# Kernel optimization log

Hardware: AMD Instinct MI355X
Metric: run time of the kernel (lower is better)

## Reference

```python
import jax, jax.numpy as jnp
import numpy as np

N_NODES = 50000
NEG_SLOPE_ATT = 0.2   # PyG GATConv default LeakyReLU slope for attention logits
NEG_SLOPE_ACT = 0.01  # nn.LeakyReLU default between layers


def _add_self_loops(src, dst, n):
    loop = jnp.arange(n, dtype=src.dtype)
    return jnp.concatenate([src, loop]), jnp.concatenate([dst, loop])


def gat_conv(x, W, a_src, a_dst, b, src, dst, n):
    # x: [N, Cin], W: [Cin, Cout], a_src/a_dst: [Cout], b: [Cout]
    h = x @ W                                   # [N, Cout]
    alpha_src = h @ a_src                       # [N]
    alpha_dst = h @ a_dst                       # [N]
    e = jax.nn.leaky_relu(alpha_src[src] + alpha_dst[dst], NEG_SLOPE_ATT)  # [E]
    # segment softmax over incoming edges of each dst node
    m = jax.ops.segment_max(e, dst, num_segments=n)      # [N]
    ex = jnp.exp(e - m[dst])                              # [E]
    s = jax.ops.segment_sum(ex, dst, num_segments=n)      # [N] (>0: self-loops)
    alpha = ex / s[dst]                                   # [E]
    out = jax.ops.segment_sum(h[src] * alpha[:, None], dst, num_segments=n)
    return out + b


def setup_inputs() -> dict:
    key = jax.random.key(0)
    ks = jax.random.split(key, 20)
    n, e = N_NODES, 800000
    cin, h1, h2, cout = 64, 128, 64, 32
    d = {
        "x": jax.random.normal(ks[0], (n, cin), jnp.float32),
        "edge_index": jax.random.randint(ks[1], (2, e), 0, n, jnp.int64),
    }
    dims = [(cin, h1), (h1, h2), (h2, h1), (h1, cout)]
    for i, (ci, co) in enumerate(dims, 1):
        g = 1.0 / np.sqrt(ci)
        d[f"W{i}"] = jax.random.normal(ks[2 + 4 * i], (ci, co), jnp.float32) * g
        d[f"a{i}s"] = jax.random.normal(ks[3 + 4 * i], (co,), jnp.float32) * 0.1
        d[f"a{i}d"] = jax.random.normal(ks[4 + 4 * i], (co,), jnp.float32) * 0.1
        d[f"b{i}"] = jnp.zeros((co,), jnp.float32)
    return d


def reference(x, edge_index, W1, a1s, a1d, b1, W2, a2s, a2d, b2,
              W3, a3s, a3d, b3, W4, a4s, a4d, b4):
    n = x.shape[0]
    src, dst = _add_self_loops(edge_index[0], edge_index[1], n)
    act = lambda t: jax.nn.leaky_relu(t, NEG_SLOPE_ACT)
    h = act(gat_conv(x, W1, a1s, a1d, b1, src, dst, n))
    # dropout is identity at inference
    h = act(gat_conv(h, W2, a2s, a2d, b2, src, dst, n))
    h = act(gat_conv(h, W3, a3s, a3d, b3, src, dst, n))
    return gat_conv(h, W4, a4s, a4d, b4, src, dst, n)
```

## Files before the change

### kernel.cpp

```cpp
#include <hip/hip_runtime.h>

#define NEG_ATT 0.2f


__global__ __launch_bounds__(256) void count_k(const int* __restrict__ dst, int* cnt, int E, int step) {
    int part = blockIdx.x & 7;
    int i = (blockIdx.x >> 3) * 256 + threadIdx.x;
    int lo = part * step, hi = lo + step;
    if (i < E) {
        int d = dst[i];
        if (d >= lo && d < hi) atomicAdd(&cnt[d], 1);
    }
}

__global__ __launch_bounds__(256) void scan_block_k(const int* __restrict__ cnt, int* rowp, int* bsum, int N) {
    __shared__ int s[256];
    int t = threadIdx.x;
    int i = blockIdx.x * 256 + t;
    s[t] = (i < N) ? cnt[i] + 1 : 0;
    __syncthreads();
    #pragma unroll
    for (int off = 1; off < 256; off <<= 1) {
        int v = (t >= off) ? s[t - off] : 0;
        __syncthreads();
        s[t] += v;
        __syncthreads();
    }
    if (i < N) rowp[i + 1] = s[t];
    if (t == 255) bsum[blockIdx.x] = s[255];
}

__global__ void scan_bsum_k(int* bsum, int nb) {
    __shared__ int s[256];
    int t = threadIdx.x;
    s[t] = (t < nb) ? bsum[t] : 0;
    __syncthreads();
    if (t == 0) {
        int run = 0;
        for (int i = 0; i < nb; i++) { int v = s[i]; s[i] = run; run += v; }
    }
    __syncthreads();
    if (t < nb) bsum[t] = s[t];
}

__global__ __launch_bounds__(256) void add_off_k(int* rowp, const int* __restrict__ bsum, int* cnt, int N) {
    int i = blockIdx.x * 256 + threadIdx.x;
    if (i < N) { rowp[i + 1] += bsum[blockIdx.x]; cnt[i] = 0; }
    if (i == 0) rowp[0] = 0;
}

__global__ __launch_bounds__(256) void scatter_k(const int* __restrict__ src, const int* __restrict__ dst,
                                                 const int* __restrict__ rowp, int* cnt,
                                                 int* __restrict__ col, int E, int N, int step) {
    int part = blockIdx.x & 7;
    int i = (blockIdx.x >> 3) * 256 + threadIdx.x;
    int lo = part * step, hi = lo + step;
    if (i < E) {
        int d = dst[i];
        if (d >= lo && d < hi) {
            int p = rowp[d] + atomicAdd(&cnt[d], 1);
            col[p] = src[i];
        }
    } else if (i < E + N) {
        int d = i - E;
        if (d >= lo && d < hi) col[rowp[d + 1] - 1] = d;
    }
}


__global__ __launch_bounds__(256) void setup_k(int* cnt, int N, int NB,
                                               const float* __restrict__ W1, const float* __restrict__ a1s,
                                               const float* __restrict__ a1d, const float* __restrict__ W3,
                                               const float* __restrict__ a3s, const float* __restrict__ a3d,
                                               float* __restrict__ wa ) {
    int b = blockIdx.x;
    if (b < NB) {
        int i = b * 256 + threadIdx.x;
        if (i < N) cnt[i] = 0;
    } else {
        int t = threadIdx.x;
        int ci = t & 63;
        int which = t >> 6;
        const float* W = (which < 2) ? W1 : W3;
        const float* a = (which == 0) ? a1s : (which == 1) ? a1d : (which == 2) ? a3s : a3d;
        float s = 0.f;
        for (int co = 0; co < 128; ++co) s += W[ci * 128 + co] * a[co];
        wa[t] = s;
    }
}


__global__ __launch_bounds__(256) void gemv_k(const float* __restrict__ X, const float* __restrict__ was,
                                              const float* __restrict__ wad, float* __restrict__ as_,
                                              float* __restrict__ ad_, int N) {
    int wid  = (blockIdx.x * 256 + threadIdx.x) >> 6;
    int lane = threadIdx.x & 63;
    if (wid >= N) return;
    float xv = X[(size_t)wid * 64 + lane];
    float s1 = xv * was[lane];
    float s2 = xv * wad[lane];
    #pragma unroll
    for (int off = 32; off; off >>= 1) {
        s1 += __shfl_xor(s1, off);
        s2 += __shfl_xor(s2, off);
    }
    if (lane == 0) { as_[wid] = s1; ad_[wid] = s2; }
}


template <int CIN, int COUT, bool ATT, bool BIASACT>
__global__ __launch_bounds__(256) void gemm_k(const float* __restrict__ X, const float* __restrict__ W,
                                              const float* __restrict__ a_s, const float* __restrict__ a_d,
                                              const float* __restrict__ bias,
                                              float* __restrict__ H, float* __restrict__ as_,
                                              float* __restrict__ ad_, int N) {
    constexpr int RB  = (CIN == 128 && COUT == 64) ? 32 : 64;
    constexpr int NCT = COUT / 4;
    constexpr int NRT = 256 / NCT;
    constexpr int RT  = RB / NRT;
    constexpr int XP  = CIN + 4;
    __shared__ float Xs[RB][XP];
    __shared__ float Ws[CIN][COUT];
    int tid  = threadIdx.x;
    int row0 = blockIdx.x * RB;

    for (int i = tid; i < CIN * COUT / 4; i += 256)
        *(float4*)&((float*)Ws)[i * 4] = *(const float4*)&W[i * 4];
    for (int i = tid; i < RB * CIN / 4; i += 256) {
        int r = i / (CIN / 4), k4 = i % (CIN / 4);
        int gr = row0 + r;
        float4 v = {0.f, 0.f, 0.f, 0.f};
        if (gr < N) v = *(const float4*)&X[(size_t)gr * CIN + k4 * 4];
        *(float4*)&Xs[r][k4 * 4] = v;
    }
    __syncthreads();

    int ct = tid % NCT;
    int rt = tid / NCT;
    float acc[RT][4] = {};
    for (int k = 0; k < CIN; k += 4) {
        float4 w0 = *(float4*)&Ws[k][ct * 4];
        float4 w1 = *(float4*)&Ws[k + 1][ct * 4];
        float4 w2 = *(float4*)&Ws[k + 2][ct * 4];
        float4 w3 = *(float4*)&Ws[k + 3][ct * 4];
        #pragma unroll
        for (int i = 0; i < RT; ++i) {
            float4 xv = *(float4*)&Xs[rt + i * NRT][k];
            acc[i][0] += xv.x * w0.x + xv.y * w1.x + xv.z * w2.x + xv.w * w3.x;
            acc[i][1] += xv.x * w0.y + xv.y * w1.y + xv.z * w2.y + xv.w * w3.y;
            acc[i][2] += xv.x * w0.z + xv.y * w1.z + xv.z * w2.z + xv.w * w3.z;
            acc[i][3] += xv.x * w0.w + xv.y * w1.w + xv.z * w2.w + xv.w * w3.w;
        }
    }

    float asv[4], adv[4], bv[4];
    #pragma unroll
    for (int j = 0; j < 4; ++j) {
        if (ATT) { asv[j] = a_s[ct * 4 + j]; adv[j] = a_d[ct * 4 + j]; }
        if (BIASACT) bv[j] = bias[ct * 4 + j];
    }

    #pragma unroll
    for (int i = 0; i < RT; ++i) {
        int gr = row0 + rt + i * NRT;
        if (BIASACT) {
            #pragma unroll
            for (int j = 0; j < 4; ++j) {
                float v = acc[i][j] + bv[j];
                acc[i][j] = v > 0.f ? v : 0.01f * v;
            }
        }
        float s1 = 0.f, s2 = 0.f;
        if (ATT) {
            s1 = acc[i][0] * asv[0] + acc[i][1] * asv[1] + acc[i][2] * asv[2] + acc[i][3] * asv[3];
            s2 = acc[i][0] * adv[0] + acc[i][1] * adv[1] + acc[i][2] * adv[2] + acc[i][3] * adv[3];
            #pragma unroll
            for (int off = 1; off < NCT; off <<= 1) {
                s1 += __shfl_xor(s1, off);
                s2 += __shfl_xor(s2, off);
            }
        }
        if (gr < N) {
            float4 o = {acc[i][0], acc[i][1], acc[i][2], acc[i][3]};
            *(float4*)&H[(size_t)gr * COUT + ct * 4] = o;
            if (ATT && ct == 0) { as_[gr] = s1; ad_[gr] = s2; }
        }
    }
}


template <int C, int MODE>
__global__ __launch_bounds__(256) void agg_k(const float* __restrict__ H, const float* __restrict__ as_,
                                             const float* __restrict__ ad_, const int* __restrict__ rowp,
                                             const int* __restrict__ col, const float* __restrict__ bias,
                                             const float* __restrict__ was, const float* __restrict__ wad,
                                             float* __restrict__ out, float* __restrict__ oas,
                                             float* __restrict__ oad, int N) {
    __shared__ int2 sw[4][64];
    int wid  = (blockIdx.x * 256 + threadIdx.x) >> 6;
    int lane = threadIdx.x & 63;
    int wvi  = threadIdx.x >> 6;
    if (wid >= N) return;
    float adi = ad_[wid];
    int beg = rowp[wid], end = rowp[wid + 1];
    float denom = 0.f;
    float a0 = 0.f, a1 = 0.f, a2 = 0.f, a3 = 0.f;
    const int sub = lane >> 5;
    const int c32 = lane & 31;

    auto g16 = [&](int j) {
        float hv[16], wv[16];
        #pragma unroll
        for (int u = 0; u < 16; ++u) {
            int2 p = sw[wvi][j + u];
            wv[u] = __int_as_float(p.y);
            hv[u] = H[(p.x << 6) | lane];
        }
        #pragma unroll
        for (int u = 0; u < 16; u += 4) {
            a0 += wv[u] * hv[u]; a1 += wv[u + 1] * hv[u + 1];
            a2 += wv[u + 2] * hv[u + 2]; a3 += wv[u + 3] * hv[u + 3];
        }
    };
    auto g8 = [&](int j) {
        float hv[8], wv[8];
        #pragma unroll
        for (int u = 0; u < 8; ++u) {
            int2 p = sw[wvi][j + u];
            wv[u] = __int_as_float(p.y);
            hv[u] = H[(p.x << 6) | lane];
        }
        #pragma unroll
        for (int u = 0; u < 8; u += 4) {
            a0 += wv[u] * hv[u]; a1 += wv[u + 1] * hv[u + 1];
            a2 += wv[u + 2] * hv[u + 2]; a3 += wv[u + 3] * hv[u + 3];
        }
    };
    auto g4 = [&](int j) {
        float hv[4], wv[4];
        #pragma unroll
        for (int u = 0; u < 4; ++u) {
            int2 p = sw[wvi][j + u];
            wv[u] = __int_as_float(p.y);
            hv[u] = H[(p.x << 6) | lane];
        }
        a0 += wv[0] * hv[0]; a1 += wv[1] * hv[1];
        a2 += wv[2] * hv[2]; a3 += wv[3] * hv[3];
    };
    auto g16_32 = [&](int j) {
        float hv[8], wv[8];
        #pragma unroll
        for (int u = 0; u < 8; ++u) {
            int2 p = sw[wvi][j + 2 * u + sub];
            wv[u] = __int_as_float(p.y);
            hv[u] = H[(p.x << 5) | c32];
        }
        #pragma unroll
        for (int u = 0; u < 8; u += 4) {
            a0 += wv[u] * hv[u]; a1 += wv[u + 1] * hv[u + 1];
            a2 += wv[u + 2] * hv[u + 2]; a3 += wv[u + 3] * hv[u + 3];
        }
    };
    auto g8_32 = [&](int j) {
        float hv[4], wv[4];
        #pragma unroll
        for (int u = 0; u < 4; ++u) {
            int2 p = sw[wvi][j + 2 * u + sub];
            wv[u] = __int_as_float(p.y);
            hv[u] = H[(p.x << 5) | c32];
        }
        a0 += wv[0] * hv[0]; a1 += wv[1] * hv[1];
        a2 += wv[2] * hv[2]; a3 += wv[3] * hv[3];
    };

    for (int base = beg; base < end; base += 64) {
        int cnt = end - base;
        if (cnt > 64) cnt = 64;
        int s_l = 0; float w_l = 0.f;
        if (lane < cnt) {
            s_l = col[base + lane];
            float e = as_[s_l] + adi;
            e = e > 0.f ? e : NEG_ATT * e;
            w_l = __expf(e);
        }
        denom += w_l;
        sw[wvi][lane] = make_int2(s_l, __float_as_int(w_l));

        int j = 0;
        if (C == 64) {
            for (; j + 16 <= cnt; j += 16) g16(j);
            int rem = cnt - j;
            if (rem > 8) g16(j);
            else if (rem > 4) g8(j);
            else if (rem > 0) g4(j);
        } else {
            for (; j + 16 <= cnt; j += 16) g16_32(j);
            int rem = cnt - j;
            if (rem > 8) g16_32(j);
            else if (rem > 0) g8_32(j);
        }
    }

    float acc = (a0 + a1) + (a2 + a3);
    #pragma unroll
    for (int off = 32; off; off >>= 1) denom += __shfl_xor(denom, off);
    if (C == 32) acc += __shfl_xor(acc, 32);

    float inv = 1.f / denom;
    float v = acc * inv;
    if (MODE == 1) {
        v += bias[lane];
        v = v > 0.f ? v : 0.01f * v;
        out[((size_t)wid << 6) | lane] = v;
        float s1 = v * was[lane];
        float s2 = v * wad[lane];
        #pragma unroll
        for (int off = 32; off; off >>= 1) {
            s1 += __shfl_xor(s1, off);
            s2 += __shfl_xor(s2, off);
        }
        if (lane == 0) { oas[wid] = s1; oad[wid] = s2; }
    } else if (MODE == 2) {
        if (lane < 32) out[((size_t)wid << 5) | c32] = v + bias[c32];
    } else {
        out[((size_t)wid << 6) | lane] = v;
    }
}


extern "C" void kernel_launch(void* const* d_in, const int* in_sizes, int n_in,
                              void* d_out, int out_size, void* d_ws, size_t ws_size,
                              hipStream_t stream) {
    const float* x  = (const float*)d_in[0];
    const int* ei   = (const int*)d_in[1];
    const float* W1 = (const float*)d_in[2];
    const float* a1s = (const float*)d_in[3];
    const float* a1d = (const float*)d_in[4];
    const float* b1  = (const float*)d_in[5];
    const float* W2 = (const float*)d_in[6];
    const float* a2s = (const float*)d_in[7];
    const float* a2d = (const float*)d_in[8];
    const float* b2  = (const float*)d_in[9];
    const float* W3 = (const float*)d_in[10];
    const float* a3s = (const float*)d_in[11];
    const float* a3d = (const float*)d_in[12];
    const float* b3  = (const float*)d_in[13];
    const float* W4 = (const float*)d_in[14];
    const float* a4s = (const float*)d_in[15];
    const float* a4d = (const float*)d_in[16];
    const float* b4  = (const float*)d_in[17];

    const int N = in_sizes[0] / 64;
    const int E = in_sizes[1] / 2;
    const int ET = E + N;
    const int* src = ei;
    const int* dst = ei + E;

    float* bufA = (float*)d_ws;
    float* bufB = bufA + (size_t)N * 128;
    float* asA  = bufB + (size_t)N * 128;
    float* adA  = asA + N;
    float* asB  = adA + N;
    float* adB  = asB + N;
    float* wa   = adB + N;
    int* cnt    = (int*)(wa + 256);
    int* rowp   = cnt + N;
    int* col    = rowp + N + 1;
    int* bsum   = col + ET;

    const int NB = (N + 255) / 256;
    const int STEP = (N + 7) / 8;

    setup_k<<<NB + 1, 256, 0, stream>>>(cnt, N, NB, W1, a1s, a1d, W3, a3s, a3d, wa);
    float* wa1s = wa, *wa1d = wa + 64, *wa3s = wa + 128, *wa3d = wa + 192;

    count_k<<<((E + 255) / 256) * 8, 256, 0, stream>>>(dst, cnt, E, STEP);
    scan_block_k<<<NB, 256, 0, stream>>>(cnt, rowp, bsum, N);
    scan_bsum_k<<<1, 256, 0, stream>>>(bsum, NB);
    add_off_k<<<NB, 256, 0, stream>>>(rowp, bsum, cnt, N);
    scatter_k<<<((ET + 255) / 256) * 8, 256, 0, stream>>>(src, dst, rowp, cnt, col, E, N, STEP);

    const int NWAVE = (N * 64 + 255) / 256;

    gemv_k<<<NWAVE, 256, 0, stream>>>(x, wa1s, wa1d, asA, adA, N);
    agg_k<64, 0><<<NWAVE, 256, 0, stream>>>(x, asA, adA, rowp, col, nullptr, nullptr, nullptr,
                                            bufA, nullptr, nullptr, N);
    gemm_k<64, 128, false, true><<<(N + 63) / 64, 256, 0, stream>>>(bufA, W1, nullptr, nullptr, b1,
                                                                    bufB, nullptr, nullptr, N);

    gemm_k<128, 64, true, false><<<(N + 31) / 32, 256, 0, stream>>>(bufB, W2, a2s, a2d, nullptr,
                                                                    bufA, asB, adB, N);
    agg_k<64, 1><<<NWAVE, 256, 0, stream>>>(bufA, asB, adB, rowp, col, b2, wa3s, wa3d,
                                            bufB, asA, adA, N);

    agg_k<64, 0><<<NWAVE, 256, 0, stream>>>(bufB, asA, adA, rowp, col, nullptr, nullptr, nullptr,
                                            bufA, nullptr, nullptr, N);
    gemm_k<64, 128, false, true><<<(N + 63) / 64, 256, 0, stream>>>(bufA, W3, nullptr, nullptr, b3,
                                                                    bufB, nullptr, nullptr, N);

    gemm_k<128, 32, true, false><<<(N + 63) / 64, 256, 0, stream>>>(bufB, W4, a4s, a4d, nullptr,
                                                                    bufA, asB, adB, N);
    agg_k<32, 2><<<NWAVE, 256, 0, stream>>>(bufA, asB, adB, rowp, col, b4, nullptr, nullptr,
                                            (float*)d_out, nullptr, nullptr, N);
}
```

Baseline: 300.2 us.

## Fuse back-to-back GEMMs, merge count with gemv, and fold bsum scan into offset kernel

Replaces the two consecutive GEMM launches (64->128 with bias+LeakyReLU, then 128->out with attention dot products) by one kernel that keeps the 128-wide intermediate in shared memory, so it is never written to or read back from global memory. The edge-count kernel and the first attention gemv are merged into a single launch, and the single-block block-sum scan is removed by having each offset block reduce the preceding block sums itself. This cuts kernel launches and the global round trip of an N x 128 buffer. In exchange the fused GEMM reloads weights in halves under extra barriers, uses more shared memory per block, and each add-offset block does a redundant reduction.

```diff
diff --git a/kernel.cpp b/kernel.cpp
--- a/kernel.cpp
+++ b/kernel.cpp
@@ -3,13 +3,31 @@
 #define NEG_ATT 0.2f
 
 
-__global__ __launch_bounds__(256) void count_k(const int* __restrict__ dst, int* cnt, int E, int step) {
-    int part = blockIdx.x & 7;
-    int i = (blockIdx.x >> 3) * 256 + threadIdx.x;
-    int lo = part * step, hi = lo + step;
-    if (i < E) {
-        int d = dst[i];
-        if (d >= lo && d < hi) atomicAdd(&cnt[d], 1);
+__global__ __launch_bounds__(256) void count_gemv_k(const int* __restrict__ dst, int* cnt, int E, int step,
+                                                    int CB, const float* __restrict__ X,
+                                                    const float* __restrict__ was, const float* __restrict__ wad,
+                                                    float* __restrict__ as_, float* __restrict__ ad_, int N) {
+    if (blockIdx.x < CB) {
+        int part = blockIdx.x & 7;
+        int i = (blockIdx.x >> 3) * 256 + threadIdx.x;
+        int lo = part * step, hi = lo + step;
+        if (i < E) {
+            int d = dst[i];
+            if (d >= lo && d < hi) atomicAdd(&cnt[d], 1);
+        }
+    } else {
+        int wid  = ((blockIdx.x - CB) * 256 + threadIdx.x) >> 6;
+        int lane = threadIdx.x & 63;
+        if (wid >= N) return;
+        float xv = X[(size_t)wid * 64 + lane];
+        float s1 = xv * was[lane];
+        float s2 = xv * wad[lane];
+        #pragma unroll
+        for (int off = 32; off; off >>= 1) {
+            s1 += __shfl_xor(s1, off);
+            s2 += __shfl_xor(s2, off);
+        }
+        if (lane == 0) { as_[wid] = s1; ad_[wid] = s2; }
     }
 }
 
@@ -30,22 +48,21 @@
     if (t == 255) bsum[blockIdx.x] = s[255];
 }
 
-__global__ void scan_bsum_k(int* bsum, int nb) {
+__global__ __launch_bounds__(256) void add_off_k(int* rowp, const int* __restrict__ bsum, int* cnt,
+                                                 int N, int nb) {
     __shared__ int s[256];
+    int b = blockIdx.x;
     int t = threadIdx.x;
-    s[t] = (t < nb) ? bsum[t] : 0;
+    s[t] = (t < b && t < nb) ? bsum[t] : 0;
     __syncthreads();
-    if (t == 0) {
-        int run = 0;
-        for (int i = 0; i < nb; i++) { int v = s[i]; s[i] = run; run += v; }
-    }
-    __syncthreads();
-    if (t < nb) bsum[t] = s[t];
-}
-
-__global__ __launch_bounds__(256) void add_off_k(int* rowp, const int* __restrict__ bsum, int* cnt, int N) {
-    int i = blockIdx.x * 256 + threadIdx.x;
-    if (i < N) { rowp[i + 1] += bsum[blockIdx.x]; cnt[i] = 0; }
+    #pragma unroll
+    for (int off = 128; off; off >>= 1) {
+        if (t < off) s[t] += s[t + off];
+        __syncthreads();
+    }
+    int prefix = s[0];
+    int i = b * 256 + t;
+    if (i < N) { rowp[i + 1] += prefix; cnt[i] = 0; }
     if (i == 0) rowp[0] = 0;
 }
 
@@ -90,100 +107,110 @@
 }
 
 
-__global__ __launch_bounds__(256) void gemv_k(const float* __restrict__ X, const float* __restrict__ was,
-                                              const float* __restrict__ wad, float* __restrict__ as_,
-                                              float* __restrict__ ad_, int N) {
-    int wid  = (blockIdx.x * 256 + threadIdx.x) >> 6;
-    int lane = threadIdx.x & 63;
-    if (wid >= N) return;
-    float xv = X[(size_t)wid * 64 + lane];
-    float s1 = xv * was[lane];
-    float s2 = xv * wad[lane];
-    #pragma unroll
-    for (int off = 32; off; off >>= 1) {
-        s1 += __shfl_xor(s1, off);
-        s2 += __shfl_xor(s2, off);
-    }
-    if (lane == 0) { as_[wid] = s1; ad_[wid] = s2; }
-}
-
-
-template <int CIN, int COUT, bool ATT, bool BIASACT>
-__global__ __launch_bounds__(256) void gemm_k(const float* __restrict__ X, const float* __restrict__ W,
-                                              const float* __restrict__ a_s, const float* __restrict__ a_d,
-                                              const float* __restrict__ bias,
-                                              float* __restrict__ H, float* __restrict__ as_,
-                                              float* __restrict__ ad_, int N) {
-    constexpr int RB  = (CIN == 128 && COUT == 64) ? 32 : 64;
-    constexpr int NCT = COUT / 4;
-    constexpr int NRT = 256 / NCT;
-    constexpr int RT  = RB / NRT;
-    constexpr int XP  = CIN + 4;
-    __shared__ float Xs[RB][XP];
-    __shared__ float Ws[CIN][COUT];
+template <int COUT>
+__global__ __launch_bounds__(256) void gemm2x_k(const float* __restrict__ X,
+                                                const float* __restrict__ W1, const float* __restrict__ b1,
+                                                const float* __restrict__ W2,
+                                                const float* __restrict__ a_s, const float* __restrict__ a_d,
+                                                float* __restrict__ H, float* __restrict__ as_,
+                                                float* __restrict__ ad_, int N) {
+    constexpr int RB = 32;
+    __shared__ float Xs[RB][68];
+    __shared__ float Wb[64][64];
+    __shared__ float H1s[RB][132];
     int tid  = threadIdx.x;
     int row0 = blockIdx.x * RB;
 
-    for (int i = tid; i < CIN * COUT / 4; i += 256)
-        *(float4*)&((float*)Ws)[i * 4] = *(const float4*)&W[i * 4];
-    for (int i = tid; i < RB * CIN / 4; i += 256) {
-        int r = i / (CIN / 4), k4 = i % (CIN / 4);
+    for (int i = tid; i < RB * 16; i += 256) {
+        int r = i / 16, k4 = i % 16;
         int gr = row0 + r;
         float4 v = {0.f, 0.f, 0.f, 0.f};
-        if (gr < N) v = *(const float4*)&X[(size_t)gr * CIN + k4 * 4];
+        if (gr < N) v = *(const float4*)&X[(size_t)gr * 64 + k4 * 4];
         *(float4*)&Xs[r][k4 * 4] = v;
     }
-    __syncthreads();
-
-    int ct = tid % NCT;
-    int rt = tid / NCT;
-    float acc[RT][4] = {};
-    for (int k = 0; k < CIN; k += 4) {
-        float4 w0 = *(float4*)&Ws[k][ct * 4];
-        float4 w1 = *(float4*)&Ws[k + 1][ct * 4];
-        float4 w2 = *(float4*)&Ws[k + 2][ct * 4];
-        float4 w3 = *(float4*)&Ws[k + 3][ct * 4];
-        #pragma unroll
-        for (int i = 0; i < RT; ++i) {
-            float4 xv = *(float4*)&Xs[rt + i * NRT][k];
-            acc[i][0] += xv.x * w0.x + xv.y * w1.x + xv.z * w2.x + xv.w * w3.x;
-            acc[i][1] += xv.x * w0.y + xv.y * w1.y + xv.z * w2.y + xv.w * w3.y;
-            acc[i][2] += xv.x * w0.z + xv.y * w1.z + xv.z * w2.z + xv.w * w3.z;
-            acc[i][3] += xv.x * w0.w + xv.y * w1.w + xv.z * w2.w + xv.w * w3.w;
-        }
-    }
-
-    float asv[4], adv[4], bv[4];
+
+    {
+        int ct = tid % 16, rt = tid / 16;
+        for (int half = 0; half < 2; ++half) {
+            __syncthreads();
+            for (int i = tid; i < 64 * 16; i += 256) {
+                int k = i / 16, c4 = i % 16;
+                *(float4*)&Wb[k][c4 * 4] = *(const float4*)&W1[k * 128 + half * 64 + c4 * 4];
+            }
+            __syncthreads();
+            float acc[2][4] = {};
+            for (int k = 0; k < 64; k += 4) {
+                float4 w0 = *(float4*)&Wb[k][ct * 4];
+                float4 w1 = *(float4*)&Wb[k + 1][ct * 4];
+                float4 w2 = *(float4*)&Wb[k + 2][ct * 4];
+                float4 w3 = *(float4*)&Wb[k + 3][ct * 4];
+                #pragma unroll
+                for (int i = 0; i < 2; ++i) {
+                    float4 xv = *(float4*)&Xs[rt + i * 16][k];
+                    acc[i][0] += xv.x * w0.x + xv.y * w1.x + xv.z * w2.x + xv.w * w3.x;
+                    acc[i][1] += xv.x * w0.y + xv.y * w1.y + xv.z * w2.y + xv.w * w3.y;
+                    acc[i][2] += xv.x * w0.z + xv.y * w1.z + xv.z * w2.z + xv.w * w3.z;
+                    acc[i][3] += xv.x * w0.w + xv.y * w1.w + xv.z * w2.w + xv.w * w3.w;
+                }
+            }
+            float4 bb = *(const float4*)&b1[half * 64 + ct * 4];
+            #pragma unroll
+            for (int i = 0; i < 2; ++i) {
+                float4 o;
+                float v0 = acc[i][0] + bb.x; o.x = v0 > 0.f ? v0 : 0.01f * v0;
+                float v1 = acc[i][1] + bb.y; o.y = v1 > 0.f ? v1 : 0.01f * v1;
+                float v2 = acc[i][2] + bb.z; o.z = v2 > 0.f ? v2 : 0.01f * v2;
+                float v3 = acc[i][3] + bb.w; o.w = v3 > 0.f ? v3 : 0.01f * v3;
+                *(float4*)&H1s[rt + i * 16][half * 64 + ct * 4] = o;
+            }
+        }
+    }
+
+    constexpr int NCTB = COUT / 4;
+    constexpr int NRTB = 256 / NCTB;
+    constexpr int RTB  = RB / NRTB;
+    int ctb = tid % NCTB, rtb = tid / NCTB;
+    float accB[RTB][4] = {};
+    for (int half = 0; half < 2; ++half) {
+        __syncthreads();
+        for (int i = tid; i < 64 * NCTB; i += 256) {
+            int k = i / NCTB, c4 = i % NCTB;
+            *(float4*)&Wb[k][c4 * 4] = *(const float4*)&W2[(half * 64 + k) * COUT + c4 * 4];
+        }
+        __syncthreads();
+        for (int k = 0; k < 64; k += 4) {
+            float4 w0 = *(float4*)&Wb[k][ctb * 4];
+            float4 w1 = *(float4*)&Wb[k + 1][ctb * 4];
+            float4 w2 = *(float4*)&Wb[k + 2][ctb * 4];
+            float4 w3 = *(float4*)&Wb[k + 3][ctb * 4];
+            #pragma unroll
+            for (int i = 0; i < RTB; ++i) {
+                float4 xv = *(float4*)&H1s[rtb + i * NRTB][half * 64 + k];
+                accB[i][0] += xv.x * w0.x + xv.y * w1.x + xv.z * w2.x + xv.w * w3.x;
+                accB[i][1] += xv.x * w0.y + xv.y * w1.y + xv.z * w2.y + xv.w * w3.y;
+                accB[i][2] += xv.x * w0.z + xv.y * w1.z + xv.z * w2.z + xv.w * w3.z;
+                accB[i][3] += xv.x * w0.w + xv.y * w1.w + xv.z * w2.w + xv.w * w3.w;
+            }
+        }
+    }
+
+    float asv[4], adv[4];
     #pragma unroll
-    for (int j = 0; j < 4; ++j) {
-        if (ATT) { asv[j] = a_s[ct * 4 + j]; adv[j] = a_d[ct * 4 + j]; }
-        if (BIASACT) bv[j] = bias[ct * 4 + j];
-    }
-
+    for (int j = 0; j < 4; ++j) { asv[j] = a_s[ctb * 4 + j]; adv[j] = a_d[ctb * 4 + j]; }
     #pragma unroll
-    for (int i = 0; i < RT; ++i) {
-        int gr = row0 + rt + i * NRT;
-        if (BIASACT) {
-            #pragma unroll
-            for (int j = 0; j < 4; ++j) {
-                float v = acc[i][j] + bv[j];
-                acc[i][j] = v > 0.f ? v : 0.01f * v;
-            }
-        }
-        float s1 = 0.f, s2 = 0.f;
-        if (ATT) {
-            s1 = acc[i][0] * asv[0] + acc[i][1] * asv[1] + acc[i][2] * asv[2] + acc[i][3] * asv[3];
-            s2 = acc[i][0] * adv[0] + acc[i][1] * adv[1] + acc[i][2] * adv[2] + acc[i][3] * adv[3];
-            #pragma unroll
-            for (int off = 1; off < NCT; off <<= 1) {
-                s1 += __shfl_xor(s1, off);
-                s2 += __shfl_xor(s2, off);
-            }
+    for (int i = 0; i < RTB; ++i) {
+        int gr = row0 + rtb + i * NRTB;
+        float s1 = accB[i][0] * asv[0] + accB[i][1] * asv[1] + accB[i][2] * asv[2] + accB[i][3] * asv[3];
+        float s2 = accB[i][0] * adv[0] + accB[i][1] * adv[1] + accB[i][2] * adv[2] + accB[i][3] * adv[3];
+        #pragma unroll
+        for (int off = 1; off < NCTB; off <<= 1) {
+            s1 += __shfl_xor(s1, off);
+            s2 += __shfl_xor(s2, off);
         }
         if (gr < N) {
-            float4 o = {acc[i][0], acc[i][1], acc[i][2], acc[i][3]};
-            *(float4*)&H[(size_t)gr * COUT + ct * 4] = o;
-            if (ATT && ct == 0) { as_[gr] = s1; ad_[gr] = s2; }
+            float4 o = {accB[i][0], accB[i][1], accB[i][2], accB[i][3]};
+            *(float4*)&H[(size_t)gr * COUT + ctb * 4] = o;
+            if (ctb == 0) { as_[gr] = s1; ad_[gr] = s2; }
         }
     }
 }
@@ -370,36 +397,32 @@
 
     const int NB = (N + 255) / 256;
     const int STEP = (N + 7) / 8;
+    const int CB = ((E + 255) / 256) * 8;
+    const int NWAVE = (N * 64 + 255) / 256;
 
     setup_k<<<NB + 1, 256, 0, stream>>>(cnt, N, NB, W1, a1s, a1d, W3, a3s, a3d, wa);
     float* wa1s = wa, *wa1d = wa + 64, *wa3s = wa + 128, *wa3d = wa + 192;
 
-    count_k<<<((E + 255) / 256) * 8, 256, 0, stream>>>(dst, cnt, E, STEP);
+    count_gemv_k<<<CB + NWAVE, 256, 0, stream>>>(dst, cnt, E, STEP, CB, x, wa1s, wa1d, asA, adA, N);
     scan_block_k<<<NB, 256, 0, stream>>>(cnt, rowp, bsum, N);
-    scan_bsum_k<<<1, 256, 0, stream>>>(bsum, NB);
-    add_off_k<<<NB, 256, 0, stream>>>(rowp, bsum, cnt, N);
+    add_off_k<<<NB, 256, 0, stream>>>(rowp, bsum, cnt, N, NB);
     scatter_k<<<((ET + 255) / 256) * 8, 256, 0, stream>>>(src, dst, rowp, cnt, col, E, N, STEP);
 
-    const int NWAVE = (N * 64 + 255) / 256;
-
-    gemv_k<<<NWAVE, 256, 0, stream>>>(x, wa1s, wa1d, asA, adA, N);
     agg_k<64, 0><<<NWAVE, 256, 0, stream>>>(x, asA, adA, rowp, col, nullptr, nullptr, nullptr,
                                             bufA, nullptr, nullptr, N);
-    gemm_k<64, 128, false, true><<<(N + 63) / 64, 256, 0, stream>>>(bufA, W1, nullptr, nullptr, b1,
-                                                                    bufB, nullptr, nullptr, N);
-
-    gemm_k<128, 64, true, false><<<(N + 31) / 32, 256, 0, stream>>>(bufB, W2, a2s, a2d, nullptr,
-                                                                    bufA, asB, adB, N);
-    agg_k<64, 1><<<NWAVE, 256, 0, stream>>>(bufA, asB, adB, rowp, col, b2, wa3s, wa3d,
-                                            bufB, asA, adA, N);
-
-    agg_k<64, 0><<<NWAVE, 256, 0, stream>>>(bufB, asA, adA, rowp, col, nullptr, nullptr, nullptr,
-                                            bufA, nullptr, nullptr, N);
-    gemm_k<64, 128, false, true><<<(N + 63) / 64, 256, 0, stream>>>(bufA, W3, nullptr, nullptr, b3,
-                                                                    bufB, nullptr, nullptr, N);
-
-    gemm_k<128, 32, true, false><<<(N + 63) / 64, 256, 0, stream>>>(bufB, W4, a4s, a4d, nullptr,
-                                                                    bufA, asB, adB, N);
+
+    gemm2x_k<64><<<(N + 31) / 32, 256, 0, stream>>>(bufA, W1, b1, W2, a2s, a2d,
+                                                    bufB, asB, adB, N);
+
+    agg_k<64, 1><<<NWAVE, 256, 0, stream>>>(bufB, asB, adB, rowp, col, b2, wa3s, wa3d,
+                                            bufA, asA, adA, N);
+
+    agg_k<64, 0><<<NWAVE, 256, 0, stream>>>(bufA, asA, adA, rowp, col, nullptr, nullptr, nullptr,
+                                            bufB, nullptr, nullptr, N);
+
+    gemm2x_k<32><<<(N + 31) / 32, 256, 0, stream>>>(bufB, W3, b3, W4, a4s, a4d,
+                                                    bufA, asB, adB, N);
+
     agg_k<32, 2><<<NWAVE, 256, 0, stream>>>(bufA, asB, adB, rowp, col, b4, nullptr, nullptr,
                                             (float*)d_out, nullptr, nullptr, N);
 }
```

After: 318.5 us. 1.06x slower.

## Fuse gemv into count kernel, merge bsum scan, add wide-tile 64x128 GEMM

Applied to the files above, without the earlier changes.

The gemv for layer-1 attention logits is folded into the degree-count kernel as extra blocks, which removes one launch. The single-thread block-sum scan kernel is dropped: each add_off block now reduces the preceding block sums itself. The 64->128 GEMMs with bias and activation move to a new kernel that computes 128 rows per block with an 8x8 register tile per thread, for more reuse per loaded value. The trade-offs are more register pressure and fewer blocks in the GEMM, plus redundant block-sum reductions in every add_off block.

```diff
diff --git a/kernel.cpp b/kernel.cpp
--- a/kernel.cpp
+++ b/kernel.cpp
@@ -3,13 +3,31 @@
 #define NEG_ATT 0.2f
 
 
-__global__ __launch_bounds__(256) void count_k(const int* __restrict__ dst, int* cnt, int E, int step) {
-    int part = blockIdx.x & 7;
-    int i = (blockIdx.x >> 3) * 256 + threadIdx.x;
-    int lo = part * step, hi = lo + step;
-    if (i < E) {
-        int d = dst[i];
-        if (d >= lo && d < hi) atomicAdd(&cnt[d], 1);
+__global__ __launch_bounds__(256) void count_gemv_k(const int* __restrict__ dst, int* cnt, int E, int step,
+                                                    int CB, const float* __restrict__ X,
+                                                    const float* __restrict__ was, const float* __restrict__ wad,
+                                                    float* __restrict__ as_, float* __restrict__ ad_, int N) {
+    if (blockIdx.x < CB) {
+        int part = blockIdx.x & 7;
+        int i = (blockIdx.x >> 3) * 256 + threadIdx.x;
+        int lo = part * step, hi = lo + step;
+        if (i < E) {
+            int d = dst[i];
+            if (d >= lo && d < hi) atomicAdd(&cnt[d], 1);
+        }
+    } else {
+        int wid  = ((blockIdx.x - CB) * 256 + threadIdx.x) >> 6;
+        int lane = threadIdx.x & 63;
+        if (wid >= N) return;
+        float xv = X[(size_t)wid * 64 + lane];
+        float s1 = xv * was[lane];
+        float s2 = xv * wad[lane];
+        #pragma unroll
+        for (int off = 32; off; off >>= 1) {
+            s1 += __shfl_xor(s1, off);
+            s2 += __shfl_xor(s2, off);
+        }
+        if (lane == 0) { as_[wid] = s1; ad_[wid] = s2; }
     }
 }
 
@@ -30,22 +48,21 @@
     if (t == 255) bsum[blockIdx.x] = s[255];
 }
 
-__global__ void scan_bsum_k(int* bsum, int nb) {
+__global__ __launch_bounds__(256) void add_off_k(int* rowp, const int* __restrict__ bsum, int* cnt,
+                                                 int N, int nb) {
     __shared__ int s[256];
+    int b = blockIdx.x;
     int t = threadIdx.x;
-    s[t] = (t < nb) ? bsum[t] : 0;
+    s[t] = (t < b && t < nb) ? bsum[t] : 0;
     __syncthreads();
-    if (t == 0) {
-        int run = 0;
-        for (int i = 0; i < nb; i++) { int v = s[i]; s[i] = run; run += v; }
-    }
-    __syncthreads();
-    if (t < nb) bsum[t] = s[t];
-}
-
-__global__ __launch_bounds__(256) void add_off_k(int* rowp, const int* __restrict__ bsum, int* cnt, int N) {
-    int i = blockIdx.x * 256 + threadIdx.x;
-    if (i < N) { rowp[i + 1] += bsum[blockIdx.x]; cnt[i] = 0; }
+    #pragma unroll
+    for (int off = 128; off; off >>= 1) {
+        if (t < off) s[t] += s[t + off];
+        __syncthreads();
+    }
+    int prefix = s[0];
+    int i = b * 256 + t;
+    if (i < N) { rowp[i + 1] += prefix; cnt[i] = 0; }
     if (i == 0) rowp[0] = 0;
 }
 
@@ -90,21 +107,64 @@
 }
 
 
-__global__ __launch_bounds__(256) void gemv_k(const float* __restrict__ X, const float* __restrict__ was,
-                                              const float* __restrict__ wad, float* __restrict__ as_,
-                                              float* __restrict__ ad_, int N) {
-    int wid  = (blockIdx.x * 256 + threadIdx.x) >> 6;
-    int lane = threadIdx.x & 63;
-    if (wid >= N) return;
-    float xv = X[(size_t)wid * 64 + lane];
-    float s1 = xv * was[lane];
-    float s2 = xv * wad[lane];
-    #pragma unroll
-    for (int off = 32; off; off >>= 1) {
-        s1 += __shfl_xor(s1, off);
-        s2 += __shfl_xor(s2, off);
-    }
-    if (lane == 0) { as_[wid] = s1; ad_[wid] = s2; }
+__global__ __launch_bounds__(256) void gemm_wide_k(const float* __restrict__ X, const float* __restrict__ W,
+                                                   const float* __restrict__ bias, float* __restrict__ H, int N) {
+    __shared__ float Xs[128][68];
+    __shared__ float Ws[64][128];
+    int tid  = threadIdx.x;
+    int row0 = blockIdx.x * 128;
+
+    for (int i = tid; i < 2048; i += 256)
+        *(float4*)&((float*)Ws)[i * 4] = *(const float4*)&W[i * 4];
+    for (int i = tid; i < 2048; i += 256) {
+        int r = i >> 4, k4 = i & 15;
+        int gr = row0 + r;
+        float4 v = {0.f, 0.f, 0.f, 0.f};
+        if (gr < N) v = *(const float4*)&X[(size_t)gr * 64 + k4 * 4];
+        *(float4*)&Xs[r][k4 * 4] = v;
+    }
+    __syncthreads();
+
+    int ct = tid & 15;
+    int rt = tid >> 4;
+    float acc[8][8] = {};
+    for (int k = 0; k < 64; k += 4) {
+        float4 w0a = *(float4*)&Ws[k][ct * 8],     w0b = *(float4*)&Ws[k][ct * 8 + 4];
+        float4 w1a = *(float4*)&Ws[k + 1][ct * 8], w1b = *(float4*)&Ws[k + 1][ct * 8 + 4];
+        float4 w2a = *(float4*)&Ws[k + 2][ct * 8], w2b = *(float4*)&Ws[k + 2][ct * 8 + 4];
+        float4 w3a = *(float4*)&Ws[k + 3][ct * 8], w3b = *(float4*)&Ws[k + 3][ct * 8 + 4];
+        #pragma unroll
+        for (int i = 0; i < 8; ++i) {
+            float4 xv = *(float4*)&Xs[rt + 16 * i][k];
+            acc[i][0] += xv.x * w0a.x + xv.y * w1a.x + xv.z * w2a.x + xv.w * w3a.x;
+            acc[i][1] += xv.x * w0a.y + xv.y * w1a.y + xv.z * w2a.y + xv.w * w3a.y;
+            acc[i][2] += xv.x * w0a.z + xv.y * w1a.z + xv.z * w2a.z + xv.w * w3a.z;
+            acc[i][3] += xv.x * w0a.w + xv.y * w1a.w + xv.z * w2a.w + xv.w * w3a.w;
+            acc[i][4] += xv.x * w0b.x + xv.y * w1b.x + xv.z * w2b.x + xv.w * w3b.x;
+            acc[i][5] += xv.x * w0b.y + xv.y * w1b.y + xv.z * w2b.y + xv.w * w3b.y;
+            acc[i][6] += xv.x * w0b.z + xv.y * w1b.z + xv.z * w2b.z + xv.w * w3b.z;
+            acc[i][7] += xv.x * w0b.w + xv.y * w1b.w + xv.z * w2b.w + xv.w * w3b.w;
+        }
+    }
+
+    float bv[8];
+    #pragma unroll
+    for (int j = 0; j < 8; ++j) bv[j] = bias[ct * 8 + j];
+
+    #pragma unroll
+    for (int i = 0; i < 8; ++i) {
+        int gr = row0 + rt + 16 * i;
+        if (gr < N) {
+            float o[8];
+            #pragma unroll
+            for (int j = 0; j < 8; ++j) {
+                float v = acc[i][j] + bv[j];
+                o[j] = v > 0.f ? v : 0.01f * v;
+            }
+            *(float4*)&H[(size_t)gr * 128 + ct * 8]     = *(float4*)&o[0];
+            *(float4*)&H[(size_t)gr * 128 + ct * 8 + 4] = *(float4*)&o[4];
+        }
+    }
 }
 
 
@@ -370,23 +430,20 @@
 
     const int NB = (N + 255) / 256;
     const int STEP = (N + 7) / 8;
+    const int CB = ((E + 255) / 256) * 8;
+    const int NWAVE = (N * 64 + 255) / 256;
 
     setup_k<<<NB + 1, 256, 0, stream>>>(cnt, N, NB, W1, a1s, a1d, W3, a3s, a3d, wa);
     float* wa1s = wa, *wa1d = wa + 64, *wa3s = wa + 128, *wa3d = wa + 192;
 
-    count_k<<<((E + 255) / 256) * 8, 256, 0, stream>>>(dst, cnt, E, STEP);
+    count_gemv_k<<<CB + NWAVE, 256, 0, stream>>>(dst, cnt, E, STEP, CB, x, wa1s, wa1d, asA, adA, N);
     scan_block_k<<<NB, 256, 0, stream>>>(cnt, rowp, bsum, N);
-    scan_bsum_k<<<1, 256, 0, stream>>>(bsum, NB);
-    add_off_k<<<NB, 256, 0, stream>>>(rowp, bsum, cnt, N);
+    add_off_k<<<NB, 256, 0, stream>>>(rowp, bsum, cnt, N, NB);
     scatter_k<<<((ET + 255) / 256) * 8, 256, 0, stream>>>(src, dst, rowp, cnt, col, E, N, STEP);
 
-    const int NWAVE = (N * 64 + 255) / 256;
-
-    gemv_k<<<NWAVE, 256, 0, stream>>>(x, wa1s, wa1d, asA, adA, N);
     agg_k<64, 0><<<NWAVE, 256, 0, stream>>>(x, asA, adA, rowp, col, nullptr, nullptr, nullptr,
                                             bufA, nullptr, nullptr, N);
-    gemm_k<64, 128, false, true><<<(N + 63) / 64, 256, 0, stream>>>(bufA, W1, nullptr, nullptr, b1,
-                                                                    bufB, nullptr, nullptr, N);
+    gemm_wide_k<<<(N + 127) / 128, 256, 0, stream>>>(bufA, W1, b1, bufB, N);
 
     gemm_k<128, 64, true, false><<<(N + 31) / 32, 256, 0, stream>>>(bufB, W2, a2s, a2d, nullptr,
                                                                     bufA, asB, adB, N);
@@ -395,8 +452,7 @@
 
     agg_k<64, 0><<<NWAVE, 256, 0, stream>>>(bufB, asA, adA, rowp, col, nullptr, nullptr, nullptr,
                                             bufA, nullptr, nullptr, N);
-    gemm_k<64, 128, false, true><<<(N + 63) / 64, 256, 0, stream>>>(bufA, W3, nullptr, nullptr, b3,
-                                                                    bufB, nullptr, nullptr, N);
+    gemm_wide_k<<<(N + 127) / 128, 256, 0, stream>>>(bufA, W3, b3, bufB, N);
 
     gemm_k<128, 32, true, false><<<(N + 63) / 64, 256, 0, stream>>>(bufB, W4, a4s, a4d, nullptr,
                                                                     bufA, asB, adB, N);
```

Result: no change. 296.2 us (-1.3%).
